# Kernel tuning notes

Measured on AMD Instinct MI355X. Metric: run time of the kernel, lower is better.

## Reference

```python
import jax, jax.numpy as jnp
import numpy as np

N_SRC = 131072
N_DST = 65536
N_EDGES = 524288
D_IN = 128
D_OUT = 128


def setup_inputs() -> dict:
    key = jax.random.key(0)
    k1, k2, k3, k4, k5 = jax.random.split(key, 5)
    feat = jax.random.normal(k1, (N_SRC, D_IN), dtype=jnp.float32)
    # xavier_uniform-ish scale for the two projections
    lim = float(np.sqrt(6.0 / (D_IN + D_OUT))) * np.sqrt(2.0)
    W_self = jax.random.uniform(k2, (D_IN, D_OUT), jnp.float32, -lim, lim)
    W_neigh = jax.random.uniform(k3, (D_IN, D_OUT), jnp.float32, -lim, lim)
    b_self = jnp.zeros((D_OUT,), jnp.float32)
    b_neigh = jnp.zeros((D_OUT,), jnp.float32)
    src_idx = jax.random.randint(k4, (N_EDGES,), 0, N_SRC, dtype=jnp.int32)
    dst_idx = jnp.sort(jax.random.randint(k5, (N_EDGES,), 0, N_DST, dtype=jnp.int32))
    return {
        "feat": feat,
        "W_self": W_self,
        "b_self": b_self,
        "W_neigh": W_neigh,
        "b_neigh": b_neigh,
        "src_idx": src_idx,
        "dst_idx": dst_idx,
        "num_row": N_DST,
    }


def reference(feat, W_self, b_self, W_neigh, b_neigh, src_idx, dst_idx, num_row):
    # h_self: destination-node features (first num_row rows)
    h_self = feat[:num_row, :]                              # [num_row, D_IN]
    # csrmm: mean aggregation of source neighbor features per destination row
    gathered = feat[src_idx]                                # [E, D_IN]
    neigh_sum = jax.ops.segment_sum(gathered, dst_idx, num_segments=num_row)
    deg = jax.ops.segment_sum(jnp.ones_like(dst_idx, dtype=feat.dtype), dst_idx,
                              num_segments=num_row)
    h_neigh = neigh_sum / jnp.maximum(deg, 1.0)[:, None]    # [num_row, D_IN]
    # dual linear projections
    rst = (h_self @ W_self + b_self) + (h_neigh @ W_neigh + b_neigh)
    return rst
```

## Files before the change

### kernel.cpp

```cpp
#include <hip/hip_runtime.h>
#include <hip/hip_bf16.h>

#define N_SRC   131072
#define N_DST   65536
#define D       128

typedef __bf16 bf16x8 __attribute__((ext_vector_type(8)));
typedef float  f32x4  __attribute__((ext_vector_type(4)));

#define CONV_BLOCKS 8192
#define W_BLOCKS    64

__global__ __launch_bounds__(256) void prep_kernel(
    const float* __restrict__ feat,
    const int*   __restrict__ dst, int n_edges, int n_bnd_blocks,
    const float* __restrict__ W_self, const float* __restrict__ W_neigh,
    __bf16* __restrict__ feat_bf,
    int*    __restrict__ row_start,
    __bf16* __restrict__ Wt_self, __bf16* __restrict__ Wt_neigh)
{
    const int b = blockIdx.x;
    const int t = threadIdx.x;

    if (b < CONV_BLOCKS) {
        const size_t i0 = ((size_t)b * 256 + t) * 8;
        const float4 a0 = *(const float4*)&feat[i0];
        const float4 a1 = *(const float4*)&feat[i0 + 4];
        bf16x8 o;
        o[0] = (__bf16)a0.x; o[1] = (__bf16)a0.y; o[2] = (__bf16)a0.z; o[3] = (__bf16)a0.w;
        o[4] = (__bf16)a1.x; o[5] = (__bf16)a1.y; o[6] = (__bf16)a1.z; o[7] = (__bf16)a1.w;
        *(bf16x8*)&feat_bf[i0] = o;
    } else if (b < CONV_BLOCKS + n_bnd_blocks) {
        const int e = (b - CONV_BLOCKS) * 256 + t;
        if (e < n_edges) {
            const int d    = dst[e];
            const int prev = (e == 0) ? -1 : dst[e - 1];
            for (int r = prev + 1; r <= d; ++r) row_start[r] = e;
            if (e == n_edges - 1)
                for (int r = d + 1; r <= N_DST; ++r) row_start[r] = n_edges;
        }
    } else {
        const int wb  = b - CONV_BLOCKS - n_bnd_blocks;
        const int idx = wb * 256 + t;
        const int k = idx >> 7, n = idx & 127;
        Wt_self [n * D + k] = (__bf16)W_self [k * D + n];
        Wt_neigh[n * D + k] = (__bf16)W_neigh[k * D + n];
    }
}

__global__ __launch_bounds__(256) void neigh_kernel(
    const __bf16* __restrict__ feat_bf,
    const int*    __restrict__ src,
    const int*    __restrict__ row_start,
    __bf16*       __restrict__ h_neigh)
{
    const int g    = threadIdx.x >> 4;
    const int lane = threadIdx.x & 15;
    const int row  = blockIdx.x * 16 + g;
    const int s0   = row_start[row];
    const int s1   = row_start[row + 1];
    const int co   = lane * 8;

    float acc[8] = {0.f, 0.f, 0.f, 0.f, 0.f, 0.f, 0.f, 0.f};

    for (int base = s0; base < s1; base += 8) {
        int idx[8];
        #pragma unroll
        for (int j = 0; j < 8; ++j) {
            const int e = base + j;
            idx[j] = src[e < s1 ? e : s1 - 1];
        }
        bf16x8 v[8];
        #pragma unroll
        for (int j = 0; j < 8; ++j)
            v[j] = *(const bf16x8*)&feat_bf[(size_t)idx[j] * D + co];
        #pragma unroll
        for (int j = 0; j < 8; ++j) {
            const float m = (base + j < s1) ? 1.0f : 0.0f;
            #pragma unroll
            for (int c = 0; c < 8; ++c)
                acc[c] = fmaf(m, (float)v[j][c], acc[c]);
        }
    }

    const float inv = 1.0f / fmaxf((float)(s1 - s0), 1.0f);
    bf16x8 o;
    #pragma unroll
    for (int c = 0; c < 8; ++c) o[c] = (__bf16)(acc[c] * inv);
    *(bf16x8*)&h_neigh[(size_t)row * D + co] = o;
}

#define MREP 2

__global__ __launch_bounds__(256) void gemm_kernel(
    const __bf16* __restrict__ feat_bf,
    const __bf16* __restrict__ h_neigh,
    const __bf16* __restrict__ Wt_self,
    const __bf16* __restrict__ Wt_neigh,
    const float*  __restrict__ b_self,
    const float*  __restrict__ b_neigh,
    float*        __restrict__ out)
{
    const int t    = threadIdx.x;
    const int w    = t >> 6;
    const int l    = t & 63;
    const int m16  = l & 15;
    const int quad = l >> 4;
    const int kb   = quad * 8;
    const int rowbase = blockIdx.x * (64 * MREP) + w * (16 * MREP);

    f32x4 acc[MREP][8];
    #pragma unroll
    for (int rp = 0; rp < MREP; ++rp)
        #pragma unroll
        for (int nb = 0; nb < 8; ++nb)
            acc[rp][nb] = (f32x4){0.f, 0.f, 0.f, 0.f};

    const __bf16* __restrict__ Aptr[2] = {feat_bf, h_neigh};
    const __bf16* __restrict__ Wptr[2] = {Wt_self, Wt_neigh};

    #pragma unroll
    for (int p = 0; p < 2; ++p) {
        const __bf16* __restrict__ A = Aptr[p];
        const __bf16* __restrict__ W = Wptr[p];
        #pragma unroll
        for (int ks = 0; ks < 4; ++ks) {
            bf16x8 afrag[MREP];
            #pragma unroll
            for (int rp = 0; rp < MREP; ++rp)
                afrag[rp] = *(const bf16x8*)&A[(size_t)(rowbase + rp * 16 + m16) * D + ks * 32 + kb];
            #pragma unroll
            for (int nb = 0; nb < 8; ++nb) {
                const bf16x8 bfrag = *(const bf16x8*)&W[(size_t)(nb * 16 + m16) * D + ks * 32 + kb];
                #pragma unroll
                for (int rp = 0; rp < MREP; ++rp)
                    acc[rp][nb] = __builtin_amdgcn_mfma_f32_16x16x32_bf16(
                        afrag[rp], bfrag, acc[rp][nb], 0, 0, 0);
            }
        }
    }

    #pragma unroll
    for (int nb = 0; nb < 8; ++nb) {
        const int col  = nb * 16 + m16;
        const float bias = b_self[col] + b_neigh[col];
        #pragma unroll
        for (int rp = 0; rp < MREP; ++rp) {
            const int orow0 = rowbase + rp * 16 + quad * 4;
            #pragma unroll
            for (int r = 0; r < 4; ++r)
                out[(size_t)(orow0 + r) * D + col] = acc[rp][nb][r] + bias;
        }
    }
}

extern "C" void kernel_launch(void* const* d_in, const int* in_sizes, int n_in,
                              void* d_out, int out_size, void* d_ws, size_t ws_size,
                              hipStream_t stream)
{
    const float* feat    = (const float*)d_in[0];
    const float* W_self  = (const float*)d_in[1];
    const float* b_self  = (const float*)d_in[2];
    const float* W_neigh = (const float*)d_in[3];
    const float* b_neigh = (const float*)d_in[4];
    const int*   src_idx = (const int*)d_in[5];
    const int*   dst_idx = (const int*)d_in[6];
    const int n_edges = in_sizes[5];

    char* ws = (char*)d_ws;
    __bf16* feat_bf  = (__bf16*)ws;
    __bf16* h_neigh  = feat_bf + (size_t)N_SRC * D;
    int*    row_start = (int*)(h_neigh + (size_t)N_DST * D);
    __bf16* Wt_self  = (__bf16*)(row_start + N_DST + 16);
    __bf16* Wt_neigh = Wt_self + D * D;

    const int n_bnd = (n_edges + 255) / 256;
    prep_kernel<<<CONV_BLOCKS + n_bnd + W_BLOCKS, 256, 0, stream>>>(
        feat, dst_idx, n_edges, n_bnd, W_self, W_neigh,
        feat_bf, row_start, Wt_self, Wt_neigh);

    neigh_kernel<<<N_DST / 16, 256, 0, stream>>>(feat_bf, src_idx, row_start, h_neigh);

    gemm_kernel<<<N_DST / (64 * MREP), 256, 0, stream>>>(
        feat_bf, h_neigh, Wt_self, Wt_neigh, b_self, b_neigh, (float*)d_out);
}
```

Before: 164.8 us.

## Fuse neighbor mean aggregation into GEMM kernel via swizzled LDS tile

```diff
diff --git a/kernel.cpp b/kernel.cpp
--- a/kernel.cpp
+++ b/kernel.cpp
@@ -48,66 +48,73 @@
     }
 }
 
-__global__ __launch_bounds__(256) void neigh_kernel(
+#define MTILE 128
+#define MREP  2
+
+__global__ __launch_bounds__(256) void fused_kernel(
     const __bf16* __restrict__ feat_bf,
     const int*    __restrict__ src,
     const int*    __restrict__ row_start,
-    __bf16*       __restrict__ h_neigh)
-{
-    const int g    = threadIdx.x >> 4;
-    const int lane = threadIdx.x & 15;
-    const int row  = blockIdx.x * 16 + g;
-    const int s0   = row_start[row];
-    const int s1   = row_start[row + 1];
-    const int co   = lane * 8;
-
-    float acc[8] = {0.f, 0.f, 0.f, 0.f, 0.f, 0.f, 0.f, 0.f};
-
-    for (int base = s0; base < s1; base += 8) {
-        int idx[8];
-        #pragma unroll
-        for (int j = 0; j < 8; ++j) {
-            const int e = base + j;
-            idx[j] = src[e < s1 ? e : s1 - 1];
-        }
-        bf16x8 v[8];
-        #pragma unroll
-        for (int j = 0; j < 8; ++j)
-            v[j] = *(const bf16x8*)&feat_bf[(size_t)idx[j] * D + co];
-        #pragma unroll
-        for (int j = 0; j < 8; ++j) {
-            const float m = (base + j < s1) ? 1.0f : 0.0f;
-            #pragma unroll
-            for (int c = 0; c < 8; ++c)
-                acc[c] = fmaf(m, (float)v[j][c], acc[c]);
-        }
-    }
-
-    const float inv = 1.0f / fmaxf((float)(s1 - s0), 1.0f);
-    bf16x8 o;
-    #pragma unroll
-    for (int c = 0; c < 8; ++c) o[c] = (__bf16)(acc[c] * inv);
-    *(bf16x8*)&h_neigh[(size_t)row * D + co] = o;
-}
-
-#define MREP 2
-
-__global__ __launch_bounds__(256) void gemm_kernel(
-    const __bf16* __restrict__ feat_bf,
-    const __bf16* __restrict__ h_neigh,
     const __bf16* __restrict__ Wt_self,
     const __bf16* __restrict__ Wt_neigh,
     const float*  __restrict__ b_self,
     const float*  __restrict__ b_neigh,
     float*        __restrict__ out)
 {
-    const int t    = threadIdx.x;
+    __shared__ __align__(16) __bf16 hs[MTILE * D];
+    char* hsb = (char*)hs;
+
+    const int t     = threadIdx.x;
+    const int tile0 = blockIdx.x * MTILE;
+
+    {
+        const int g    = t >> 4;
+        const int lane = t & 15;
+        const int cb   = lane * 16;
+
+        #pragma unroll
+        for (int rr = 0; rr < MTILE / 16; ++rr) {
+            const int rloc = rr * 16 + g;
+            const int s0 = row_start[tile0 + rloc];
+            const int s1 = row_start[tile0 + rloc + 1];
+
+            float acc[8] = {0.f, 0.f, 0.f, 0.f, 0.f, 0.f, 0.f, 0.f};
+
+            for (int base = s0; base < s1; base += 8) {
+                int idx[8];
+                #pragma unroll
+                for (int j = 0; j < 8; ++j) {
+                    const int e = base + j;
+                    idx[j] = src[e < s1 ? e : s1 - 1];
+                }
+                bf16x8 v[8];
+                #pragma unroll
+                for (int j = 0; j < 8; ++j)
+                    v[j] = *(const bf16x8*)((const char*)feat_bf + (size_t)idx[j] * (D * 2) + cb);
+                #pragma unroll
+                for (int j = 0; j < 8; ++j) {
+                    const float m = (base + j < s1) ? 1.0f : 0.0f;
+                    #pragma unroll
+                    for (int c = 0; c < 8; ++c)
+                        acc[c] = fmaf(m, (float)v[j][c], acc[c]);
+                }
+            }
+
+            const float inv = 1.0f / fmaxf((float)(s1 - s0), 1.0f);
+            bf16x8 o;
+            #pragma unroll
+            for (int c = 0; c < 8; ++c) o[c] = (__bf16)(acc[c] * inv);
+            *(bf16x8*)(hsb + rloc * 256 + (cb ^ ((rloc & 7) << 4))) = o;
+        }
+    }
+
     const int w    = t >> 6;
     const int l    = t & 63;
     const int m16  = l & 15;
     const int quad = l >> 4;
     const int kb   = quad * 8;
-    const int rowbase = blockIdx.x * (64 * MREP) + w * (16 * MREP);
+    const int rowloc0 = w * (16 * MREP);
+    const int rowbase = tile0 + rowloc0;
 
     f32x4 acc[MREP][8];
     #pragma unroll
@@ -116,27 +123,40 @@
         for (int nb = 0; nb < 8; ++nb)
             acc[rp][nb] = (f32x4){0.f, 0.f, 0.f, 0.f};
 
-    const __bf16* __restrict__ Aptr[2] = {feat_bf, h_neigh};
-    const __bf16* __restrict__ Wptr[2] = {Wt_self, Wt_neigh};
-
-    #pragma unroll
-    for (int p = 0; p < 2; ++p) {
-        const __bf16* __restrict__ A = Aptr[p];
-        const __bf16* __restrict__ W = Wptr[p];
-        #pragma unroll
-        for (int ks = 0; ks < 4; ++ks) {
-            bf16x8 afrag[MREP];
+    #pragma unroll
+    for (int ks = 0; ks < 4; ++ks) {
+        bf16x8 afrag[MREP];
+        #pragma unroll
+        for (int rp = 0; rp < MREP; ++rp)
+            afrag[rp] = *(const bf16x8*)&feat_bf[(size_t)(rowbase + rp * 16 + m16) * D + ks * 32 + kb];
+        #pragma unroll
+        for (int nb = 0; nb < 8; ++nb) {
+            const bf16x8 bfrag = *(const bf16x8*)&Wt_self[(size_t)(nb * 16 + m16) * D + ks * 32 + kb];
             #pragma unroll
             for (int rp = 0; rp < MREP; ++rp)
-                afrag[rp] = *(const bf16x8*)&A[(size_t)(rowbase + rp * 16 + m16) * D + ks * 32 + kb];
-            #pragma unroll
-            for (int nb = 0; nb < 8; ++nb) {
-                const bf16x8 bfrag = *(const bf16x8*)&W[(size_t)(nb * 16 + m16) * D + ks * 32 + kb];
-                #pragma unroll
-                for (int rp = 0; rp < MREP; ++rp)
-                    acc[rp][nb] = __builtin_amdgcn_mfma_f32_16x16x32_bf16(
-                        afrag[rp], bfrag, acc[rp][nb], 0, 0, 0);
-            }
+                acc[rp][nb] = __builtin_amdgcn_mfma_f32_16x16x32_bf16(
+                    afrag[rp], bfrag, acc[rp][nb], 0, 0, 0);
+        }
+    }
+
+    __syncthreads();
+
+    #pragma unroll
+    for (int ks = 0; ks < 4; ++ks) {
+        bf16x8 afrag[MREP];
+        #pragma unroll
+        for (int rp = 0; rp < MREP; ++rp) {
+            const int rloc  = rowloc0 + rp * 16 + m16;
+            const int cbyte = (ks * 32 + kb) * 2;
+            afrag[rp] = *(const bf16x8*)(hsb + rloc * 256 + (cbyte ^ ((rloc & 7) << 4)));
+        }
+        #pragma unroll
+        for (int nb = 0; nb < 8; ++nb) {
+            const bf16x8 bfrag = *(const bf16x8*)&Wt_neigh[(size_t)(nb * 16 + m16) * D + ks * 32 + kb];
+            #pragma unroll
+            for (int rp = 0; rp < MREP; ++rp)
+                acc[rp][nb] = __builtin_amdgcn_mfma_f32_16x16x32_bf16(
+                    afrag[rp], bfrag, acc[rp][nb], 0, 0, 0);
         }
     }
 
@@ -169,8 +189,7 @@
 
     char* ws = (char*)d_ws;
     __bf16* feat_bf  = (__bf16*)ws;
-    __bf16* h_neigh  = feat_bf + (size_t)N_SRC * D;
-    int*    row_start = (int*)(h_neigh + (size_t)N_DST * D);
+    int*    row_start = (int*)(feat_bf + (size_t)N_SRC * D);
     __bf16* Wt_self  = (__bf16*)(row_start + N_DST + 16);
     __bf16* Wt_neigh = Wt_self + D * D;
 
@@ -179,8 +198,7 @@
         feat, dst_idx, n_edges, n_bnd, W_self, W_neigh,
         feat_bf, row_start, Wt_self, Wt_neigh);
 
-    neigh_kernel<<<N_DST / 16, 256, 0, stream>>>(feat_bf, src_idx, row_start, h_neigh);
-
-    gemm_kernel<<<N_DST / (64 * MREP), 256, 0, stream>>>(
-        feat_bf, h_neigh, Wt_self, Wt_neigh, b_self, b_neigh, (float*)d_out);
+    fused_kernel<<<N_DST / MTILE, 256, 0, stream>>>(
+        feat_bf, src_idx, row_start, Wt_self, Wt_neigh,
+        b_self, b_neigh, (float*)d_out);
 }
```

New measurement: 160.1 us. -2.9%, faster.
